# Performance work log

Measured on AMD Instinct MI355X. Metric: run time of the kernel, lower is better.

Reference implementation:

```python
import jax, jax.numpy as jnp
import numpy as np

B, T, C, H = 512, 256, 384, 64  # batch, seq (block_size), n_embd, head_size
SCALE = C ** 0.5  # NOTE: source multiplies by C**0.5 (faithful to original)


def setup_inputs() -> dict:
    key = jax.random.key(0)
    kx, kq, kk, kv = jax.random.split(key, 4)
    lim = 1.0 / np.sqrt(C)
    return {
        "x": jax.random.normal(kx, (B, T, C), dtype=jnp.float32),
        "Wq": jax.random.uniform(kq, (C, H), jnp.float32, -lim, lim),
        "Wk": jax.random.uniform(kk, (C, H), jnp.float32, -lim, lim),
        "Wv": jax.random.uniform(kv, (C, H), jnp.float32, -lim, lim),
    }


def reference(x, Wq, Wk, Wv):
    q = jnp.einsum("btc,ch->bth", x, Wq)
    k = jnp.einsum("btc,ch->bth", x, Wk)
    v = jnp.einsum("btc,ch->bth", x, Wv)
    wei = jnp.einsum("bth,bsh->bts", q, k) * SCALE  # [B,T,T]
    causal = jnp.tril(jnp.ones((T, T), dtype=bool))
    wei = jnp.where(causal, wei, -jnp.inf)
    wei = jax.nn.softmax(wei, axis=-1)
    # dropout is identity in eval mode
    out = jnp.einsum("bts,bsh->bth", wei, v)
    return out
```

## Files before the change

kernel.cpp:

```cpp
#include <hip/hip_runtime.h>
#include <math.h>

#define B_ 512
#define T_ 256
#define C_ 384
#define H_ 64

typedef __attribute__((ext_vector_type(8))) short bf16x8;
typedef __attribute__((ext_vector_type(4))) float f32x4;

#define MFMA16(a, b, c) __builtin_amdgcn_mfma_f32_16x16x32_bf16((a), (b), (c), 0, 0, 0)

#define SM_KHI   0u
#define SM_KLO   36864u
#define SM_VT    73728u
#define SM_WQH   73728u
#define SM_WQL   78848u
#define SM_WKH   83968u
#define SM_WKL   89088u
#define SM_WVH   94208u
#define SM_WVL   99328u
#define SM_XREG  107520u
#define SM_XH    107520u
#define SM_XL    128000u
#define SM_QS(s) (SM_XREG + (unsigned)(s)*18432u)
#define SM_PS(w) (SM_XREG + (unsigned)(w)*9216u)
#define SM_BYTES 148480u

static __device__ __forceinline__ unsigned short bhi(float x) {
    return (unsigned short)(__float_as_uint(x) >> 16);
}
static __device__ __forceinline__ unsigned short blo(float x) {
    float h = __uint_as_float((__float_as_uint(x) >> 16) << 16);
    return (unsigned short)(__float_as_uint(x - h) >> 16);
}
static __device__ __forceinline__ unsigned short brne(float x) {
    unsigned u = __float_as_uint(x);
    return (unsigned short)((u + 0x7FFFu + ((u >> 16) & 1u)) >> 16);
}
static __device__ __forceinline__ unsigned pk_hi(float a, float b) {
    return (unsigned)bhi(a) | ((unsigned)bhi(b) << 16);
}
static __device__ __forceinline__ unsigned pk_lo(float a, float b) {
    return (unsigned)blo(a) | ((unsigned)blo(b) << 16);
}

__global__ __launch_bounds__(256, 1)
void head_mfma(const float* __restrict__ x,
               const float* __restrict__ Wq,
               const float* __restrict__ Wk,
               const float* __restrict__ Wv,
               float* __restrict__ out)
{
    __shared__ __align__(16) unsigned char sm[SM_BYTES];

    const int tid  = threadIdx.x;
    const int b    = blockIdx.x;
    const int w    = tid >> 6;
    const int lane = tid & 63;
    const int l15  = lane & 15;
    const int quad = lane >> 4;
    const int w64  = w * 64;

    f32x4 qac[4][4], kac[4][4], vac[4][4];
    #pragma unroll
    for (int mt = 0; mt < 4; ++mt)
        #pragma unroll
        for (int nt = 0; nt < 4; ++nt) {
            f32x4 z = {0.f, 0.f, 0.f, 0.f};
            qac[mt][nt] = z; kac[mt][nt] = z; vac[mt][nt] = z;
        }

    const float* xrow = x + ((size_t)b * T_ + tid) * C_;
    const int hW  = tid >> 2;
    const int cgW = (tid & 3) * 8;

    float4 xb[8];
    float  wbq[8], wbk[8], wbv[8];
    {
        const float4* xp = (const float4*)(xrow);
        #pragma unroll
        for (int j = 0; j < 8; ++j) xb[j] = xp[j];
        const float* q0 = Wq + (size_t)cgW * H_ + hW;
        const float* k0 = Wk + (size_t)cgW * H_ + hW;
        const float* v0 = Wv + (size_t)cgW * H_ + hW;
        #pragma unroll
        for (int j = 0; j < 8; ++j) { wbq[j] = q0[j*H_]; wbk[j] = k0[j*H_]; wbv[j] = v0[j*H_]; }
    }

    #pragma unroll 1
    for (int cc = 0; cc < 12; ++cc) {
        #pragma unroll
        for (int j = 0; j < 8; ++j) {
            uint2 hh, ll;
            hh.x = pk_hi(xb[j].x, xb[j].y); hh.y = pk_hi(xb[j].z, xb[j].w);
            ll.x = pk_lo(xb[j].x, xb[j].y); ll.y = pk_lo(xb[j].z, xb[j].w);
            *(uint2*)&sm[SM_XH + (unsigned)(tid*80 + j*8)] = hh;
            *(uint2*)&sm[SM_XL + (unsigned)(tid*80 + j*8)] = ll;
        }
        {
            const unsigned wo = (unsigned)(hW*80 + (tid&3)*16);
            uint4 t;
            t.x=pk_hi(wbq[0],wbq[1]); t.y=pk_hi(wbq[2],wbq[3]); t.z=pk_hi(wbq[4],wbq[5]); t.w=pk_hi(wbq[6],wbq[7]);
            *(uint4*)&sm[SM_WQH + wo] = t;
            t.x=pk_lo(wbq[0],wbq[1]); t.y=pk_lo(wbq[2],wbq[3]); t.z=pk_lo(wbq[4],wbq[5]); t.w=pk_lo(wbq[6],wbq[7]);
            *(uint4*)&sm[SM_WQL + wo] = t;
            t.x=pk_hi(wbk[0],wbk[1]); t.y=pk_hi(wbk[2],wbk[3]); t.z=pk_hi(wbk[4],wbk[5]); t.w=pk_hi(wbk[6],wbk[7]);
            *(uint4*)&sm[SM_WKH + wo] = t;
            t.x=pk_lo(wbk[0],wbk[1]); t.y=pk_lo(wbk[2],wbk[3]); t.z=pk_lo(wbk[4],wbk[5]); t.w=pk_lo(wbk[6],wbk[7]);
            *(uint4*)&sm[SM_WKL + wo] = t;
            t.x=pk_hi(wbv[0],wbv[1]); t.y=pk_hi(wbv[2],wbv[3]); t.z=pk_hi(wbv[4],wbv[5]); t.w=pk_hi(wbv[6],wbv[7]);
            *(uint4*)&sm[SM_WVH + wo] = t;
            t.x=pk_lo(wbv[0],wbv[1]); t.y=pk_lo(wbv[2],wbv[3]); t.z=pk_lo(wbv[4],wbv[5]); t.w=pk_lo(wbv[6],wbv[7]);
            *(uint4*)&sm[SM_WVL + wo] = t;
        }
        __syncthreads();

        if (cc < 11) {
            const float4* xp = (const float4*)(xrow + (cc + 1) * 32);
            #pragma unroll
            for (int j = 0; j < 8; ++j) xb[j] = xp[j];
            const size_t c0 = (size_t)((cc + 1) * 32 + cgW) * H_ + hW;
            #pragma unroll
            for (int j = 0; j < 8; ++j) {
                wbq[j] = Wq[c0 + (size_t)j*H_];
                wbk[j] = Wk[c0 + (size_t)j*H_];
                wbv[j] = Wv[c0 + (size_t)j*H_];
            }
        }

        bf16x8 ah[4], al[4];
        #pragma unroll
        for (int mt = 0; mt < 4; ++mt) {
            const unsigned ro = (unsigned)((w64 + mt*16 + l15)*80 + quad*16);
            ah[mt] = *(const bf16x8*)&sm[SM_XH + ro];
            al[mt] = *(const bf16x8*)&sm[SM_XL + ro];
        }
#define PROJ_MAT(WTH, WTL, ACC)                                               \
        {                                                                     \
            bf16x8 bh[4], bl[4];                                              \
            _Pragma("unroll")                                                 \
            for (int nt = 0; nt < 4; ++nt) {                                  \
                const unsigned bo = (unsigned)((nt*16 + l15)*80 + quad*16);   \
                bh[nt] = *(const bf16x8*)&sm[(WTH) + bo];                     \
                bl[nt] = *(const bf16x8*)&sm[(WTL) + bo];                     \
            }                                                                 \
            _Pragma("unroll")                                                 \
            for (int mt = 0; mt < 4; ++mt)                                    \
                _Pragma("unroll")                                             \
                for (int nt = 0; nt < 4; ++nt) {                              \
                    f32x4 a = ACC[mt][nt];                                    \
                    a = MFMA16(al[mt], bh[nt], a);                            \
                    a = MFMA16(ah[mt], bl[nt], a);                            \
                    a = MFMA16(ah[mt], bh[nt], a);                            \
                    ACC[mt][nt] = a;                                          \
                }                                                             \
        }
        PROJ_MAT(SM_WQH, SM_WQL, qac)
        PROJ_MAT(SM_WKH, SM_WKL, kac)
        PROJ_MAT(SM_WVH, SM_WVL, vac)
        __syncthreads();
    }

    constexpr float SCALE = 19.595917942265423f;
    #pragma unroll
    for (int mt = 0; mt < 4; ++mt)
        #pragma unroll
        for (int nt = 0; nt < 4; ++nt) {
            const f32x4 kv = kac[mt][nt];
            const f32x4 vv = vac[mt][nt];
            #pragma unroll
            for (int r = 0; r < 4; ++r) {
                const int row = w64 + mt*16 + quad*4 + r;
                const int h   = nt*16 + l15;
                *(unsigned short*)&sm[SM_KHI + (unsigned)(row*144 + h*2)] = bhi(kv[r]);
                *(unsigned short*)&sm[SM_KLO + (unsigned)(row*144 + h*2)] = blo(kv[r]);
                *(unsigned short*)&sm[SM_VT  + (unsigned)(h*528 + row*2)] = brne(vv[r]);
            }
        }

    bf16x8 qAh[4][2], qAl[4][2];
    const int slot = w & 1;
#define Q_XPOSE()                                                             \
    {                                                                         \
        const unsigned qb = SM_QS(slot);                                      \
        _Pragma("unroll")                                                     \
        for (int mt = 0; mt < 4; ++mt)                                        \
            _Pragma("unroll")                                                 \
            for (int nt = 0; nt < 4; ++nt) {                                  \
                const f32x4 qv = qac[mt][nt];                                 \
                _Pragma("unroll")                                             \
                for (int r = 0; r < 4; ++r) {                                 \
                    const float qs = qv[r] * SCALE;                           \
                    const int rl = mt*16 + quad*4 + r;                        \
                    const int h  = nt*16 + l15;                               \
                    *(unsigned short*)&sm[qb +         (unsigned)(rl*144 + h*2)] = bhi(qs); \
                    *(unsigned short*)&sm[qb + 9216u + (unsigned)(rl*144 + h*2)] = blo(qs); \
                }                                                             \
            }                                                                 \
        _Pragma("unroll")                                                     \
        for (int mt = 0; mt < 4; ++mt)                                        \
            _Pragma("unroll")                                                 \
            for (int ks = 0; ks < 2; ++ks) {                                  \
                const unsigned qo = (unsigned)((mt*16 + l15)*144 + ks*64 + quad*16); \
                qAh[mt][ks] = *(const bf16x8*)&sm[qb + qo];                   \
                qAl[mt][ks] = *(const bf16x8*)&sm[qb + 9216u + qo];           \
            }                                                                 \
    }
    if (w < 2) Q_XPOSE();
    __syncthreads();
    if (w >= 2) Q_XPOSE();
    __syncthreads();

    f32x4 oac[4][4];
    float m_[4][4], l_[4][4];
    #pragma unroll
    for (int mt = 0; mt < 4; ++mt) {
        #pragma unroll
        for (int nt = 0; nt < 4; ++nt) { f32x4 z = {0.f,0.f,0.f,0.f}; oac[mt][nt] = z; }
        #pragma unroll
        for (int r = 0; r < 4; ++r) { m_[mt][r] = -1e30f; l_[mt][r] = 0.f; }
    }
    const unsigned pb = SM_PS(w);

    #pragma unroll 1
    for (int kb = 0; kb <= w; ++kb) {
        bf16x8 kbh[4][2], kbl[4][2];
        #pragma unroll
        for (int nt = 0; nt < 4; ++nt)
            #pragma unroll
            for (int ks = 0; ks < 2; ++ks) {
                const unsigned ko = (unsigned)((kb*64 + nt*16 + l15)*144 + ks*64 + quad*16);
                kbh[nt][ks] = *(const bf16x8*)&sm[SM_KHI + ko];
                kbl[nt][ks] = *(const bf16x8*)&sm[SM_KLO + ko];
            }
        f32x4 sac[4][4];
        #pragma unroll
        for (int mt = 0; mt < 4; ++mt)
            #pragma unroll
            for (int nt = 0; nt < 4; ++nt) {
                f32x4 a = {0.f,0.f,0.f,0.f};
                #pragma unroll
                for (int ks = 0; ks < 2; ++ks) {
                    a = MFMA16(qAl[mt][ks], kbh[nt][ks], a);
                    a = MFMA16(qAh[mt][ks], kbl[nt][ks], a);
                    a = MFMA16(qAh[mt][ks], kbh[nt][ks], a);
                }
                sac[mt][nt] = a;
            }
        if (kb == w) {
            #pragma unroll
            for (int mt = 0; mt < 4; ++mt)
                #pragma unroll
                for (int nt = 0; nt < 4; ++nt)
                    #pragma unroll
                    for (int r = 0; r < 4; ++r) {
                        const int rl = mt*16 + quad*4 + r;
                        const int kl = nt*16 + l15;
                        if (kl > rl) sac[mt][nt][r] = -1e30f;
                    }
        }
        #pragma unroll
        for (int mt = 0; mt < 4; ++mt) {
            f32x4 mx = sac[mt][0];
            #pragma unroll
            for (int nt = 1; nt < 4; ++nt) {
                #pragma unroll
                for (int r = 0; r < 4; ++r) mx[r] = fmaxf(mx[r], sac[mt][nt][r]);
            }
            #pragma unroll
            for (int r = 0; r < 4; ++r) {
                float v = mx[r];
                v = fmaxf(v, __shfl_xor(v, 1)); v = fmaxf(v, __shfl_xor(v, 2));
                v = fmaxf(v, __shfl_xor(v, 4)); v = fmaxf(v, __shfl_xor(v, 8));
                const float mnew  = fmaxf(m_[mt][r], v);
                const float alpha = __expf(m_[mt][r] - mnew);
                m_[mt][r] = mnew;
                float rs = 0.f;
                #pragma unroll
                for (int nt = 0; nt < 4; ++nt) {
                    const float p = __expf(sac[mt][nt][r] - mnew);
                    sac[mt][nt][r] = p;
                    rs += p;
                }
                rs += __shfl_xor(rs, 1); rs += __shfl_xor(rs, 2);
                rs += __shfl_xor(rs, 4); rs += __shfl_xor(rs, 8);
                l_[mt][r] = l_[mt][r] * alpha + rs;
                #pragma unroll
                for (int nt = 0; nt < 4; ++nt) oac[mt][nt][r] *= alpha;
                const int rl = mt*16 + quad*4 + r;
                #pragma unroll
                for (int nt = 0; nt < 4; ++nt)
                    *(unsigned short*)&sm[pb + (unsigned)(rl*144 + (nt*16 + l15)*2)] =
                        brne(sac[mt][nt][r]);
            }
        }
        bf16x8 pA[4][2], vB[4][2];
        #pragma unroll
        for (int mt = 0; mt < 4; ++mt)
            #pragma unroll
            for (int ks = 0; ks < 2; ++ks)
                pA[mt][ks] = *(const bf16x8*)&sm[pb + (unsigned)((mt*16 + l15)*144 + ks*64 + quad*16)];
        #pragma unroll
        for (int nt = 0; nt < 4; ++nt)
            #pragma unroll
            for (int ks = 0; ks < 2; ++ks)
                vB[nt][ks] = *(const bf16x8*)&sm[SM_VT + (unsigned)((nt*16 + l15)*528 + kb*128 + ks*64 + quad*16)];
        #pragma unroll
        for (int mt = 0; mt < 4; ++mt)
            #pragma unroll
            for (int nt = 0; nt < 4; ++nt) {
                f32x4 a = oac[mt][nt];
                a = MFMA16(pA[mt][0], vB[nt][0], a);
                a = MFMA16(pA[mt][1], vB[nt][1], a);
                oac[mt][nt] = a;
            }
    }

    float inv[4][4];
    #pragma unroll
    for (int mt = 0; mt < 4; ++mt)
        #pragma unroll
        for (int r = 0; r < 4; ++r) inv[mt][r] = 1.0f / l_[mt][r];
    float* ob = out + (size_t)b * (T_ * H_);
    #pragma unroll
    for (int mt = 0; mt < 4; ++mt)
        #pragma unroll
        for (int nt = 0; nt < 4; ++nt)
            #pragma unroll
            for (int r = 0; r < 4; ++r) {
                const int row = w64 + mt*16 + quad*4 + r;
                const int h   = nt*16 + l15;
                ob[row*64 + h] = oac[mt][nt][r] * inv[mt][r];
            }
}

extern "C" void kernel_launch(void* const* d_in, const int* in_sizes, int n_in,
                              void* d_out, int out_size, void* d_ws, size_t ws_size,
                              hipStream_t stream)
{
    const float* x  = (const float*)d_in[0];
    const float* Wq = (const float*)d_in[1];
    const float* Wk = (const float*)d_in[2];
    const float* Wv = (const float*)d_in[3];
    head_mfma<<<dim3(B_), dim3(T_), 0, stream>>>(x, Wq, Wk, Wv, (float*)d_out);
}
```

Baseline: 384.6 us.

## Use 8 waves per block with causal-balanced paired row tiles

Doubles the block to 512 threads so each wave owns two 16-row query tiles, one near the top and one near the bottom of the sequence (w and 15-w). This evens out the causal attention work across waves, which was previously skewed toward the last wave. The projection, Q transpose slots and P staging buffers are resized to match. More waves per CU can also hide latency better. The cost is more barrier participants, and the launch bound asks for 2 blocks per CU, which tightens the register budget and risks spills.

```diff
diff --git a/kernel.cpp b/kernel.cpp
--- a/kernel.cpp
+++ b/kernel.cpp
@@ -23,8 +23,8 @@
 #define SM_XREG  107520u
 #define SM_XH    107520u
 #define SM_XL    128000u
-#define SM_QS(s) (SM_XREG + (unsigned)(s)*18432u)
-#define SM_PS(w) (SM_XREG + (unsigned)(w)*9216u)
+#define SM_QS(s) (SM_XREG + (unsigned)(s)*9216u)
+#define SM_PS(w) (SM_XREG + (unsigned)(w)*2304u)
 #define SM_BYTES 148480u
 
 static __device__ __forceinline__ unsigned short bhi(float x) {
@@ -45,7 +45,7 @@
     return (unsigned)blo(a) | ((unsigned)blo(b) << 16);
 }
 
-__global__ __launch_bounds__(256, 1)
+__global__ __launch_bounds__(512, 2)
 void head_mfma(const float* __restrict__ x,
                const float* __restrict__ Wq,
                const float* __restrict__ Wk,
@@ -60,81 +60,80 @@
     const int lane = tid & 63;
     const int l15  = lane & 15;
     const int quad = lane >> 4;
-    const int w64  = w * 64;
-
-    f32x4 qac[4][4], kac[4][4], vac[4][4];
-    #pragma unroll
-    for (int mt = 0; mt < 4; ++mt)
+    const int rA   = w * 16;
+    const int rB   = 240 - w * 16;
+
+    f32x4 qac[2][4], kac[2][4], vac[2][4];
+    #pragma unroll
+    for (int mt = 0; mt < 2; ++mt)
         #pragma unroll
         for (int nt = 0; nt < 4; ++nt) {
             f32x4 z = {0.f, 0.f, 0.f, 0.f};
             qac[mt][nt] = z; kac[mt][nt] = z; vac[mt][nt] = z;
         }
 
-    const float* xrow = x + ((size_t)b * T_ + tid) * C_;
-    const int hW  = tid >> 2;
-    const int cgW = (tid & 3) * 8;
-
-    float4 xb[8];
-    float  wbq[8], wbk[8], wbv[8];
+    const int xrowi = tid >> 1;
+    const int xhalf = tid & 1;
+    const float* xrow = x + ((size_t)b * T_ + xrowi) * C_ + xhalf * 16;
+    const int hW = tid >> 3;
+    const int cg = tid & 7;
+
+    float4 xb[4];
+    float  wbq[4], wbk[4], wbv[4];
     {
         const float4* xp = (const float4*)(xrow);
         #pragma unroll
-        for (int j = 0; j < 8; ++j) xb[j] = xp[j];
-        const float* q0 = Wq + (size_t)cgW * H_ + hW;
-        const float* k0 = Wk + (size_t)cgW * H_ + hW;
-        const float* v0 = Wv + (size_t)cgW * H_ + hW;
-        #pragma unroll
-        for (int j = 0; j < 8; ++j) { wbq[j] = q0[j*H_]; wbk[j] = k0[j*H_]; wbv[j] = v0[j*H_]; }
+        for (int j = 0; j < 4; ++j) xb[j] = xp[j];
+        const float* q0 = Wq + (size_t)(cg * 4) * H_ + hW;
+        const float* k0 = Wk + (size_t)(cg * 4) * H_ + hW;
+        const float* v0 = Wv + (size_t)(cg * 4) * H_ + hW;
+        #pragma unroll
+        for (int j = 0; j < 4; ++j) { wbq[j] = q0[j*H_]; wbk[j] = k0[j*H_]; wbv[j] = v0[j*H_]; }
     }
 
     #pragma unroll 1
     for (int cc = 0; cc < 12; ++cc) {
         #pragma unroll
-        for (int j = 0; j < 8; ++j) {
+        for (int j = 0; j < 4; ++j) {
             uint2 hh, ll;
             hh.x = pk_hi(xb[j].x, xb[j].y); hh.y = pk_hi(xb[j].z, xb[j].w);
             ll.x = pk_lo(xb[j].x, xb[j].y); ll.y = pk_lo(xb[j].z, xb[j].w);
-            *(uint2*)&sm[SM_XH + (unsigned)(tid*80 + j*8)] = hh;
-            *(uint2*)&sm[SM_XL + (unsigned)(tid*80 + j*8)] = ll;
+            *(uint2*)&sm[SM_XH + (unsigned)(xrowi*80 + xhalf*32 + j*8)] = hh;
+            *(uint2*)&sm[SM_XL + (unsigned)(xrowi*80 + xhalf*32 + j*8)] = ll;
         }
         {
-            const unsigned wo = (unsigned)(hW*80 + (tid&3)*16);
-            uint4 t;
-            t.x=pk_hi(wbq[0],wbq[1]); t.y=pk_hi(wbq[2],wbq[3]); t.z=pk_hi(wbq[4],wbq[5]); t.w=pk_hi(wbq[6],wbq[7]);
-            *(uint4*)&sm[SM_WQH + wo] = t;
-            t.x=pk_lo(wbq[0],wbq[1]); t.y=pk_lo(wbq[2],wbq[3]); t.z=pk_lo(wbq[4],wbq[5]); t.w=pk_lo(wbq[6],wbq[7]);
-            *(uint4*)&sm[SM_WQL + wo] = t;
-            t.x=pk_hi(wbk[0],wbk[1]); t.y=pk_hi(wbk[2],wbk[3]); t.z=pk_hi(wbk[4],wbk[5]); t.w=pk_hi(wbk[6],wbk[7]);
-            *(uint4*)&sm[SM_WKH + wo] = t;
-            t.x=pk_lo(wbk[0],wbk[1]); t.y=pk_lo(wbk[2],wbk[3]); t.z=pk_lo(wbk[4],wbk[5]); t.w=pk_lo(wbk[6],wbk[7]);
-            *(uint4*)&sm[SM_WKL + wo] = t;
-            t.x=pk_hi(wbv[0],wbv[1]); t.y=pk_hi(wbv[2],wbv[3]); t.z=pk_hi(wbv[4],wbv[5]); t.w=pk_hi(wbv[6],wbv[7]);
-            *(uint4*)&sm[SM_WVH + wo] = t;
-            t.x=pk_lo(wbv[0],wbv[1]); t.y=pk_lo(wbv[2],wbv[3]); t.z=pk_lo(wbv[4],wbv[5]); t.w=pk_lo(wbv[6],wbv[7]);
-            *(uint4*)&sm[SM_WVL + wo] = t;
+            const unsigned wo = (unsigned)(hW*80 + cg*8);
+            uint2 t;
+            t.x = pk_hi(wbq[0],wbq[1]); t.y = pk_hi(wbq[2],wbq[3]); *(uint2*)&sm[SM_WQH + wo] = t;
+            t.x = pk_lo(wbq[0],wbq[1]); t.y = pk_lo(wbq[2],wbq[3]); *(uint2*)&sm[SM_WQL + wo] = t;
+            t.x = pk_hi(wbk[0],wbk[1]); t.y = pk_hi(wbk[2],wbk[3]); *(uint2*)&sm[SM_WKH + wo] = t;
+            t.x = pk_lo(wbk[0],wbk[1]); t.y = pk_lo(wbk[2],wbk[3]); *(uint2*)&sm[SM_WKL + wo] = t;
+            t.x = pk_hi(wbv[0],wbv[1]); t.y = pk_hi(wbv[2],wbv[3]); *(uint2*)&sm[SM_WVH + wo] = t;
+            t.x = pk_lo(wbv[0],wbv[1]); t.y = pk_lo(wbv[2],wbv[3]); *(uint2*)&sm[SM_WVL + wo] = t;
         }
         __syncthreads();
 
         if (cc < 11) {
             const float4* xp = (const float4*)(xrow + (cc + 1) * 32);
             #pragma unroll
-            for (int j = 0; j < 8; ++j) xb[j] = xp[j];
-            const size_t c0 = (size_t)((cc + 1) * 32 + cgW) * H_ + hW;
-            #pragma unroll
-            for (int j = 0; j < 8; ++j) {
+            for (int j = 0; j < 4; ++j) xb[j] = xp[j];
+            const size_t c0 = (size_t)((cc + 1) * 32 + cg * 4) * H_ + hW;
+            #pragma unroll
+            for (int j = 0; j < 4; ++j) {
                 wbq[j] = Wq[c0 + (size_t)j*H_];
                 wbk[j] = Wk[c0 + (size_t)j*H_];
                 wbv[j] = Wv[c0 + (size_t)j*H_];
             }
         }
 
-        bf16x8 ah[4], al[4];
-        #pragma unroll
-        for (int mt = 0; mt < 4; ++mt) {
-            const unsigned ro = (unsigned)((w64 + mt*16 + l15)*80 + quad*16);
-            ah[mt] = *(const bf16x8*)&sm[SM_XH + ro];
-            al[mt] = *(const bf16x8*)&sm[SM_XL + ro];
+        bf16x8 ah[2], al[2];
+        {
+            const unsigned roA = (unsigned)((rA + l15)*80 + quad*16);
+            const unsigned roB = (unsigned)((rB + l15)*80 + quad*16);
+            ah[0] = *(const bf16x8*)&sm[SM_XH + roA];
+            al[0] = *(const bf16x8*)&sm[SM_XL + roA];
+            ah[1] = *(const bf16x8*)&sm[SM_XH + roB];
+            al[1] = *(const bf16x8*)&sm[SM_XL + roB];
         }
 #define PROJ_MAT(WTH, WTL, ACC)                                               \
         {                                                                     \
@@ -146,7 +145,7 @@
                 bl[nt] = *(const bf16x8*)&sm[(WTL) + bo];                     \
             }                                                                 \
             _Pragma("unroll")                                                 \
-            for (int mt = 0; mt < 4; ++mt)                                    \
+            for (int mt = 0; mt < 2; ++mt)                                    \
                 _Pragma("unroll")                                             \
                 for (int nt = 0; nt < 4; ++nt) {                              \
                     f32x4 a = ACC[mt][nt];                                    \
@@ -164,28 +163,30 @@
 
     constexpr float SCALE = 19.595917942265423f;
     #pragma unroll
-    for (int mt = 0; mt < 4; ++mt)
+    for (int mt = 0; mt < 2; ++mt) {
+        const int r0m = mt ? rB : rA;
         #pragma unroll
         for (int nt = 0; nt < 4; ++nt) {
             const f32x4 kv = kac[mt][nt];
             const f32x4 vv = vac[mt][nt];
             #pragma unroll
             for (int r = 0; r < 4; ++r) {
-                const int row = w64 + mt*16 + quad*4 + r;
+                const int row = r0m + quad*4 + r;
                 const int h   = nt*16 + l15;
                 *(unsigned short*)&sm[SM_KHI + (unsigned)(row*144 + h*2)] = bhi(kv[r]);
                 *(unsigned short*)&sm[SM_KLO + (unsigned)(row*144 + h*2)] = blo(kv[r]);
                 *(unsigned short*)&sm[SM_VT  + (unsigned)(h*528 + row*2)] = brne(vv[r]);
             }
         }
-
-    bf16x8 qAh[4][2], qAl[4][2];
-    const int slot = w & 1;
+    }
+
+    bf16x8 qAh[2][2], qAl[2][2];
+    const int slot = w & 3;
 #define Q_XPOSE()                                                             \
     {                                                                         \
         const unsigned qb = SM_QS(slot);                                      \
         _Pragma("unroll")                                                     \
-        for (int mt = 0; mt < 4; ++mt)                                        \
+        for (int mt = 0; mt < 2; ++mt)                                        \
             _Pragma("unroll")                                                 \
             for (int nt = 0; nt < 4; ++nt) {                                  \
                 const f32x4 qv = qac[mt][nt];                                 \
@@ -195,27 +196,27 @@
                     const int rl = mt*16 + quad*4 + r;                        \
                     const int h  = nt*16 + l15;                               \
                     *(unsigned short*)&sm[qb +         (unsigned)(rl*144 + h*2)] = bhi(qs); \
-                    *(unsigned short*)&sm[qb + 9216u + (unsigned)(rl*144 + h*2)] = blo(qs); \
+                    *(unsigned short*)&sm[qb + 4608u + (unsigned)(rl*144 + h*2)] = blo(qs); \
                 }                                                             \
             }                                                                 \
         _Pragma("unroll")                                                     \
-        for (int mt = 0; mt < 4; ++mt)                                        \
+        for (int mt = 0; mt < 2; ++mt)                                        \
             _Pragma("unroll")                                                 \
             for (int ks = 0; ks < 2; ++ks) {                                  \
                 const unsigned qo = (unsigned)((mt*16 + l15)*144 + ks*64 + quad*16); \
                 qAh[mt][ks] = *(const bf16x8*)&sm[qb + qo];                   \
-                qAl[mt][ks] = *(const bf16x8*)&sm[qb + 9216u + qo];           \
+                qAl[mt][ks] = *(const bf16x8*)&sm[qb + 4608u + qo];           \
             }                                                                 \
     }
-    if (w < 2) Q_XPOSE();
+    if (w < 4) Q_XPOSE();
     __syncthreads();
-    if (w >= 2) Q_XPOSE();
+    if (w >= 4) Q_XPOSE();
     __syncthreads();
 
-    f32x4 oac[4][4];
-    float m_[4][4], l_[4][4];
-    #pragma unroll
-    for (int mt = 0; mt < 4; ++mt) {
+    f32x4 oac[2][4];
+    float m_[2][4], l_[2][4];
+    #pragma unroll
+    for (int mt = 0; mt < 2; ++mt) {
         #pragma unroll
         for (int nt = 0; nt < 4; ++nt) { f32x4 z = {0.f,0.f,0.f,0.f}; oac[mt][nt] = z; }
         #pragma unroll
@@ -223,116 +224,104 @@
     }
     const unsigned pb = SM_PS(w);
 
-    #pragma unroll 1
-    for (int kb = 0; kb <= w; ++kb) {
-        bf16x8 kbh[4][2], kbl[4][2];
-        #pragma unroll
-        for (int nt = 0; nt < 4; ++nt)
-            #pragma unroll
-            for (int ks = 0; ks < 2; ++ks) {
-                const unsigned ko = (unsigned)((kb*64 + nt*16 + l15)*144 + ks*64 + quad*16);
-                kbh[nt][ks] = *(const bf16x8*)&sm[SM_KHI + ko];
-                kbl[nt][ks] = *(const bf16x8*)&sm[SM_KLO + ko];
-            }
-        f32x4 sac[4][4];
-        #pragma unroll
-        for (int mt = 0; mt < 4; ++mt)
+    #pragma unroll
+    for (int tile = 0; tile < 2; ++tile) {
+        const int r0    = tile ? rB : rA;
+        const int kbmax = tile ? ((15 - w) >> 2) : (w >> 2);
+        #pragma unroll 1
+        for (int kb = 0; kb <= kbmax; ++kb) {
+            bf16x8 kbh[4][2], kbl[4][2];
+            #pragma unroll
+            for (int nt = 0; nt < 4; ++nt)
+                #pragma unroll
+                for (int ks = 0; ks < 2; ++ks) {
+                    const unsigned ko = (unsigned)((kb*64 + nt*16 + l15)*144 + ks*64 + quad*16);
+                    kbh[nt][ks] = *(const bf16x8*)&sm[SM_KHI + ko];
+                    kbl[nt][ks] = *(const bf16x8*)&sm[SM_KLO + ko];
+                }
+            f32x4 sac[4];
             #pragma unroll
             for (int nt = 0; nt < 4; ++nt) {
                 f32x4 a = {0.f,0.f,0.f,0.f};
                 #pragma unroll
                 for (int ks = 0; ks < 2; ++ks) {
-                    a = MFMA16(qAl[mt][ks], kbh[nt][ks], a);
-                    a = MFMA16(qAh[mt][ks], kbl[nt][ks], a);
-                    a = MFMA16(qAh[mt][ks], kbh[nt][ks], a);
+                    a = MFMA16(qAl[tile][ks], kbh[nt][ks], a);
+                    a = MFMA16(qAh[tile][ks], kbl[nt][ks], a);
+                    a = MFMA16(qAh[tile][ks], kbh[nt][ks], a);
                 }
-                sac[mt][nt] = a;
-            }
-        if (kb == w) {
-            #pragma unroll
-            for (int mt = 0; mt < 4; ++mt)
+                sac[nt] = a;
+            }
+            if (kb == kbmax) {
                 #pragma unroll
                 for (int nt = 0; nt < 4; ++nt)
                     #pragma unroll
                     for (int r = 0; r < 4; ++r) {
-                        const int rl = mt*16 + quad*4 + r;
-                        const int kl = nt*16 + l15;
-                        if (kl > rl) sac[mt][nt][r] = -1e30f;
+                        const int rg = r0 + quad*4 + r;
+                        const int kl = kb*64 + nt*16 + l15;
+                        if (kl > rg) sac[nt][r] = -1e30f;
                     }
-        }
-        #pragma unroll
-        for (int mt = 0; mt < 4; ++mt) {
-            f32x4 mx = sac[mt][0];
-            #pragma unroll
-            for (int nt = 1; nt < 4; ++nt) {
-                #pragma unroll
-                for (int r = 0; r < 4; ++r) mx[r] = fmaxf(mx[r], sac[mt][nt][r]);
             }
             #pragma unroll
             for (int r = 0; r < 4; ++r) {
-                float v = mx[r];
+                float v = fmaxf(fmaxf(sac[0][r], sac[1][r]), fmaxf(sac[2][r], sac[3][r]));
                 v = fmaxf(v, __shfl_xor(v, 1)); v = fmaxf(v, __shfl_xor(v, 2));
                 v = fmaxf(v, __shfl_xor(v, 4)); v = fmaxf(v, __shfl_xor(v, 8));
-                const float mnew  = fmaxf(m_[mt][r], v);
-                const float alpha = __expf(m_[mt][r] - mnew);
-                m_[mt][r] = mnew;
+                const float mnew  = fmaxf(m_[tile][r], v);
+                const float alpha = __expf(m_[tile][r] - mnew);
+                m_[tile][r] = mnew;
                 float rs = 0.f;
                 #pragma unroll
                 for (int nt = 0; nt < 4; ++nt) {
-                    const float p = __expf(sac[mt][nt][r] - mnew);
-                    sac[mt][nt][r] = p;
+                    const float p = __expf(sac[nt][r] - mnew);
+                    sac[nt][r] = p;
                     rs += p;
                 }
                 rs += __shfl_xor(rs, 1); rs += __shfl_xor(rs, 2);
                 rs += __shfl_xor(rs, 4); rs += __shfl_xor(rs, 8);
-                l_[mt][r] = l_[mt][r] * alpha + rs;
-                #pragma unroll
-                for (int nt = 0; nt < 4; ++nt) oac[mt][nt][r] *= alpha;
-                const int rl = mt*16 + quad*4 + r;
+                l_[tile][r] = l_[tile][r] * alpha + rs;
+                #pragma unroll
+                for (int nt = 0; nt < 4; ++nt) oac[tile][nt][r] *= alpha;
+                const int rl = quad*4 + r;
                 #pragma unroll
                 for (int nt = 0; nt < 4; ++nt)
                     *(unsigned short*)&sm[pb + (unsigned)(rl*144 + (nt*16 + l15)*2)] =
-                        brne(sac[mt][nt][r]);
-            }
-        }
-        bf16x8 pA[4][2], vB[4][2];
-        #pragma unroll
-        for (int mt = 0; mt < 4; ++mt)
+                        brne(sac[nt][r]);
+            }
+            bf16x8 pA[2], vB[4][2];
             #pragma unroll
             for (int ks = 0; ks < 2; ++ks)
-                pA[mt][ks] = *(const bf16x8*)&sm[pb + (unsigned)((mt*16 + l15)*144 + ks*64 + quad*16)];
+                pA[ks] = *(const bf16x8*)&sm[pb + (unsigned)(l15*144 + ks*64 + quad*16)];
+            #pragma unroll
+            for (int nt = 0; nt < 4; ++nt)
+                #pragma unroll
+                for (int ks = 0; ks < 2; ++ks)
+                    vB[nt][ks] = *(const bf16x8*)&sm[SM_VT + (unsigned)((nt*16 + l15)*528 + kb*128 + ks*64 + quad*16)];
+            #pragma unroll
+            for (int nt = 0; nt < 4; ++nt) {
+                f32x4 a = oac[tile][nt];
+                a = MFMA16(pA[0], vB[nt][0], a);
+                a = MFMA16(pA[1], vB[nt][1], a);
+                oac[tile][nt] = a;
+            }
+        }
+    }
+
+    float* ob = out + (size_t)b * (T_ * H_);
+    #pragma unroll
+    for (int mt = 0; mt < 2; ++mt) {
+        const int r0m = mt ? rB : rA;
+        float inv[4];
+        #pragma unroll
+        for (int r = 0; r < 4; ++r) inv[r] = 1.0f / l_[mt][r];
         #pragma unroll
         for (int nt = 0; nt < 4; ++nt)
             #pragma unroll
-            for (int ks = 0; ks < 2; ++ks)
-                vB[nt][ks] = *(const bf16x8*)&sm[SM_VT + (unsigned)((nt*16 + l15)*528 + kb*128 + ks*64 + quad*16)];
-        #pragma unroll
-        for (int mt = 0; mt < 4; ++mt)
-            #pragma unroll
-            for (int nt = 0; nt < 4; ++nt) {
-                f32x4 a = oac[mt][nt];
-                a = MFMA16(pA[mt][0], vB[nt][0], a);
-                a = MFMA16(pA[mt][1], vB[nt][1], a);
-                oac[mt][nt] = a;
-            }
-    }
-
-    float inv[4][4];
-    #pragma unroll
-    for (int mt = 0; mt < 4; ++mt)
-        #pragma unroll
-        for (int r = 0; r < 4; ++r) inv[mt][r] = 1.0f / l_[mt][r];
-    float* ob = out + (size_t)b * (T_ * H_);
-    #pragma unroll
-    for (int mt = 0; mt < 4; ++mt)
-        #pragma unroll
-        for (int nt = 0; nt < 4; ++nt)
-            #pragma unroll
             for (int r = 0; r < 4; ++r) {
-                const int row = w64 + mt*16 + quad*4 + r;
+                const int row = r0m + quad*4 + r;
                 const int h   = nt*16 + l15;
-                ob[row*64 + h] = oac[mt][nt][r] * inv[mt][r];
-            }
+                ob[row*64 + h] = oac[mt][nt][r] * inv[r];
+            }
+    }
 }
 
 extern "C" void kernel_launch(void* const* d_in, const int* in_sizes, int n_in,
@@ -343,5 +332,5 @@
     const float* Wq = (const float*)d_in[1];
     const float* Wk = (const float*)d_in[2];
     const float* Wv = (const float*)d_in[3];
-    head_mfma<<<dim3(B_), dim3(T_), 0, stream>>>(x, Wq, Wk, Wv, (float*)d_out);
-}
+    head_mfma<<<dim3(B_), dim3(512), 0, stream>>>(x, Wq, Wk, Wv, (float*)d_out);
+}
```

Measured after the change: 330.0 us. -14.2%, faster.
